# Optimization experiments

Measured on AMD Instinct MI355X. Metric: run time of the kernel, lower is better.

## Reference

```python
import jax, jax.numpy as jnp
import numpy as np

N, E = 50000, 800000
F_IN, HID, H, LBL = 512, 16, 8, 40
HC = HID * H  # 128
BN_EPS = 1e-5
ELU_ALPHA = 0.2
NEG_SLOPE = 0.2


def setup_inputs() -> dict:
    key = jax.random.key(0)
    ks = jax.random.split(key, 32)
    inp = {}
    inp['x'] = jax.random.normal(ks[0], (N, F_IN), dtype=jnp.float32)
    inp['edge_index'] = jax.random.randint(ks[1], (2, E), 0, N, dtype=jnp.int32)
    # layer 0: F_IN -> (H, HID), concat
    inp['W0'] = jax.random.normal(ks[2], (F_IN, HC), dtype=jnp.float32) * 0.05
    inp['as0'] = jax.random.normal(ks[3], (H, HID), dtype=jnp.float32) * 0.1
    inp['ad0'] = jax.random.normal(ks[4], (H, HID), dtype=jnp.float32) * 0.1
    inp['b0'] = jnp.zeros((HC,), jnp.float32)
    inp['g0'] = jnp.ones((HC,), jnp.float32)
    inp['be0'] = jnp.zeros((HC,), jnp.float32)
    inp['rm0'] = jnp.zeros((HC,), jnp.float32)
    inp['rv0'] = jnp.ones((HC,), jnp.float32)
    # layer 1: HC -> (H, HID), concat
    inp['W1'] = jax.random.normal(ks[5], (HC, HC), dtype=jnp.float32) * 0.1
    inp['as1'] = jax.random.normal(ks[6], (H, HID), dtype=jnp.float32) * 0.1
    inp['ad1'] = jax.random.normal(ks[7], (H, HID), dtype=jnp.float32) * 0.1
    inp['b1'] = jnp.zeros((HC,), jnp.float32)
    inp['g1'] = jnp.ones((HC,), jnp.float32)
    inp['be1'] = jnp.zeros((HC,), jnp.float32)
    inp['rm1'] = jnp.zeros((HC,), jnp.float32)
    inp['rv1'] = jnp.ones((HC,), jnp.float32)
    # layer 2: HC -> (1, LBL), mean (concat=False)
    inp['W2'] = jax.random.normal(ks[8], (HC, LBL), dtype=jnp.float32) * 0.1
    inp['as2'] = jax.random.normal(ks[9], (1, LBL), dtype=jnp.float32) * 0.1
    inp['ad2'] = jax.random.normal(ks[10], (1, LBL), dtype=jnp.float32) * 0.1
    inp['b2'] = jnp.zeros((LBL,), jnp.float32)
    return inp


def _gat_conv(xf, src, dst, W, a_src, a_dst, b, heads, out_ch, concat):
    # PyG GATConv (eval): linear -> per-head attn logits -> segment softmax over dst -> scatter-add
    n = xf.shape[0]
    h = (xf @ W).reshape(n, heads, out_ch)            # [N,H,C]
    alpha_s = jnp.einsum('nhc,hc->nh', h, a_src)      # [N,H]
    alpha_d = jnp.einsum('nhc,hc->nh', h, a_dst)
    e = jax.nn.leaky_relu(alpha_s[src] + alpha_d[dst], NEG_SLOPE)  # [Etot,H]
    m = jax.ops.segment_max(e, dst, num_segments=n)
    e = jnp.exp(e - m[dst])
    s = jax.ops.segment_sum(e, dst, num_segments=n)
    alpha = e / (s[dst] + 1e-16)                      # [Etot,H]
    msg = alpha[:, :, None] * h[src]                  # [Etot,H,C]
    out = jax.ops.segment_sum(msg, dst, num_segments=n)  # [N,H,C]
    out = out.reshape(n, heads * out_ch) if concat else out.mean(axis=1)
    return out + b


def _bn_elu(xf, g, be, rm, rv):
    y = (xf - rm) * (g * jax.lax.rsqrt(rv + BN_EPS)) + be
    return jnp.where(y > 0, y, ELU_ALPHA * jnp.expm1(y))


def reference(x, edge_index, W0, as0, ad0, b0, g0, be0, rm0, rv0,
              W1, as1, ad1, b1, g1, be1, rm1, rv1, W2, as2, ad2, b2):
    n = x.shape[0]
    # add self-loops (PyG GATConv default add_self_loops=True)
    loops = jnp.arange(n, dtype=edge_index.dtype)
    src = jnp.concatenate([edge_index[0], loops])
    dst = jnp.concatenate([edge_index[1], loops])
    h = _gat_conv(x, src, dst, W0, as0, ad0, b0, H, HID, True)
    h = _bn_elu(h, g0, be0, rm0, rv0)
    h = _gat_conv(h, src, dst, W1, as1, ad1, b1, H, HID, True)
    h = _bn_elu(h, g1, be1, rm1, rv1)
    out = _gat_conv(h, src, dst, W2, as2, ad2, b2, 1, LBL, False)
    return out
```

## Files before the change

### kernel.cpp

```cpp
#include <hip/hip_runtime.h>
#include <hip/hip_bf16.h>
#include <cstdint>
#include <cstddef>

#define NN 50000
#define EE 800000
#define FIN 512
#define HIDC 16
#define NH 8
#define HCH 128
#define NLBL 40
#define NLBLP 48
#define ETOT (EE + NN)
#define NEG_SLOPE 0.2f
#define ELU_A 0.2f
#define BN_EPS 1e-5f
#define SCH 8192
#define NCHK 7

typedef __attribute__((ext_vector_type(8))) short bf16x8;
typedef __attribute__((ext_vector_type(4))) short bf16x4;
typedef __attribute__((ext_vector_type(4))) float f32x4;

__device__ inline short f2b(float f) {
    __hip_bfloat16 h = __float2bfloat16(f);
    return *reinterpret_cast<short*>(&h);
}
__device__ inline float blo(unsigned int u) {
    union { unsigned int u; float f; } v; v.u = u << 16; return v.f;
}
__device__ inline float bhi(unsigned int u) {
    union { unsigned int u; float f; } v; v.u = u & 0xffff0000u; return v.f;
}

__global__ __launch_bounds__(256) void k_prep(const float* __restrict__ W0, short* __restrict__ Wt0,
                                              const float* __restrict__ W1, short* __restrict__ Wt1,
                                              const float* __restrict__ W2, short* __restrict__ Wt2,
                                              const int* __restrict__ ei, int* __restrict__ deg,
                                              const float* __restrict__ x, short* __restrict__ xc)
{
    int b = blockIdx.x;
    int tid = threadIdx.x;
    if (b < 256) {
        int idx = b * 256 + tid;
        int n = idx >> 9, k = idx & 511;
        Wt0[idx] = f2b(W0[(size_t)k * HCH + n]);
        return;
    }
    b -= 256;
    if (b < 64) {
        int idx = b * 256 + tid;
        int n = idx >> 7, k = idx & 127;
        Wt1[idx] = f2b(W1[(size_t)k * HCH + n]);
        return;
    }
    b -= 64;
    if (b < 24) {
        int idx = b * 256 + tid;
        int n = idx >> 7, k = idx & 127;
        Wt2[idx] = f2b(n < NLBL ? W2[(size_t)k * NLBL + n] : 0.f);
        return;
    }
    b -= 24;
    if (b < 3321) {
        int e = b * 256 + tid;
        if (e < ETOT) {
            int dst = (e < EE) ? ei[EE + e] : (e - EE);
            atomicAdd(&deg[dst], 1);
        }
        return;
    }
    b -= 3321;
    {
        int t = b * 256 + tid;
        if (t < NN * (FIN / 8)) {
            int idx = t * 8;
            int row = idx >> 9;
            int ko  = idx & 511;
            int c   = ko >> 7;
            int kk  = ko & 127;
            const float4* p = (const float4*)(x + (size_t)row * FIN + ko);
            float4 v0 = p[0], v1 = p[1];
            bf16x8 w;
            w[0] = f2b(v0.x); w[1] = f2b(v0.y); w[2] = f2b(v0.z); w[3] = f2b(v0.w);
            w[4] = f2b(v1.x); w[5] = f2b(v1.y); w[6] = f2b(v1.z); w[7] = f2b(v1.w);
            *(bf16x8*)(xc + ((size_t)c * NN + row) * 128 + kk) = w;
        }
    }
}

__global__ __launch_bounds__(1024) void k_scan1(const int* __restrict__ deg,
                                                int* __restrict__ row_ptr,
                                                int* __restrict__ tot)
{
    __shared__ int sm[1024];
    int b = blockIdx.x, tid = threadIdx.x;
    int i0 = b * SCH + tid * 8;
    int v[8];
    int s = 0;
    #pragma unroll
    for (int j = 0; j < 8; ++j) {
        int i = i0 + j;
        v[j] = (i < NN) ? deg[i] : 0;
        s += v[j];
    }
    sm[tid] = s;
    __syncthreads();
    for (int ofs = 1; ofs < 1024; ofs <<= 1) {
        int t = (tid >= ofs) ? sm[tid - ofs] : 0;
        __syncthreads();
        sm[tid] += t;
        __syncthreads();
    }
    int excl = sm[tid] - s;
    #pragma unroll
    for (int j = 0; j < 8; ++j) {
        int i = i0 + j;
        if (i < NN) row_ptr[i] = excl;
        excl += v[j];
    }
    if (tid == 1023) tot[b] = sm[1023];
}

__global__ __launch_bounds__(64) void k_scan2(const int* __restrict__ tot,
                                              int* __restrict__ totp,
                                              int* __restrict__ row_ptr)
{
    if (threadIdx.x == 0) {
        int run = 0;
        for (int i = 0; i < NCHK; ++i) { totp[i] = run; run += tot[i]; }
        row_ptr[NN] = run;
    }
}

__global__ __launch_bounds__(256) void k_scan3(int* __restrict__ row_ptr,
                                               int* __restrict__ cursor,
                                               const int* __restrict__ totp)
{
    int i = blockIdx.x * 256 + threadIdx.x;
    if (i < NN) {
        int v = row_ptr[i] + totp[i / SCH];
        row_ptr[i] = v;
        cursor[i] = v;
    }
}

__global__ __launch_bounds__(256) void k_scatter(const int* __restrict__ ei,
                                                 int* __restrict__ cursor,
                                                 int* __restrict__ csr_src)
{
    int e = blockIdx.x * blockDim.x + threadIdx.x;
    if (e >= ETOT) return;
    int src, dst;
    if (e < EE) { src = ei[e]; dst = ei[EE + e]; }
    else        { src = dst = e - EE; }
    int pos = atomicAdd(&cursor[dst], 1);
    csr_src[pos] = src;
}

template<int KDIM, bool CHUNK_MAJOR>
__global__ __launch_bounds__(512, 4) void k_gemm2(const short* __restrict__ Ab,
                                                  const short* __restrict__ Wt,
                                                  short* __restrict__ C,
                                                  int M,
                                                  const float* __restrict__ a_s,
                                                  const float* __restrict__ a_d,
                                                  float* __restrict__ as_o,
                                                  float* __restrict__ ad_o)
{
    constexpr int KCH  = 128;
    constexpr int NCH  = KDIM / KCH;
    constexpr int LROW = KCH + 8;
    __shared__ short As[64 * LROW];
    __shared__ short Bs[128 * LROW];

    const int tid  = threadIdx.x;
    const int wv   = tid >> 6;
    const int lane = tid & 63;
    const int quad = lane >> 4;
    const int col  = lane & 15;
    const int wr   = wv >> 1;
    const int wn   = wv & 1;
    const int rowbase = blockIdx.x * 64;

    bf16x8 pab[2];
    bf16x8 pb[4];

    auto loadA = [&](int c) {
        #pragma unroll
        for (int r = 0; r < 2; ++r) {
            int gr = rowbase + r * 32 + (tid >> 4);
            gr = gr < M ? gr : M - 1;
            size_t base = CHUNK_MAJOR ? ((size_t)c * M + gr) * KCH
                                      : (size_t)gr * KDIM + (size_t)c * KCH;
            pab[r] = *(const bf16x8*)(Ab + base + (tid & 15) * 8);
        }
    };
    auto loadB = [&](int c) {
        #pragma unroll
        for (int r = 0; r < 4; ++r) {
            int n = r * 32 + (tid >> 4);
            pb[r] = *(const bf16x8*)(Wt + (size_t)n * KDIM + (size_t)c * KCH + (tid & 15) * 8);
        }
    };
    auto writeAB = [&]() {
        #pragma unroll
        for (int r = 0; r < 2; ++r) {
            int row = r * 32 + (tid >> 4);
            *(bf16x8*)(As + row * LROW + (tid & 15) * 8) = pab[r];
        }
        #pragma unroll
        for (int r = 0; r < 4; ++r) {
            int n = r * 32 + (tid >> 4);
            *(bf16x8*)(Bs + n * LROW + (tid & 15) * 8) = pb[r];
        }
    };

    f32x4 acc[4];
    #pragma unroll
    for (int t = 0; t < 4; ++t) acc[t] = (f32x4){0.f, 0.f, 0.f, 0.f};

    loadA(0); loadB(0);

    for (int c = 0; c < NCH; ++c) {
        writeAB();
        __syncthreads();
        if (c + 1 < NCH) { loadA(c + 1); loadB(c + 1); }
        #pragma unroll
        for (int s = 0; s < KCH / 32; ++s) {
            bf16x8 af = *(const bf16x8*)(As + (wr * 16 + col) * LROW + s * 32 + quad * 8);
            #pragma unroll
            for (int t = 0; t < 4; ++t) {
                bf16x8 bf = *(const bf16x8*)(Bs + (wn * 64 + t * 16 + col) * LROW + s * 32 + quad * 8);
                acc[t] = __builtin_amdgcn_mfma_f32_16x16x32_bf16(af, bf, acc[t], 0, 0, 0);
            }
        }
        if (c + 1 < NCH) __syncthreads();
    }

    const int mb = rowbase + wr * 16 + quad * 4;

    #pragma unroll
    for (int t = 0; t < 4; ++t) {
        int cc = wn * 64 + t * 16 + col;
        #pragma unroll
        for (int r = 0; r < 4; ++r) {
            int m = mb + r;
            if (m < M) C[(size_t)m * HCH + cc] = f2b(acc[t][r]);
        }
    }

    #pragma unroll
    for (int t = 0; t < 4; ++t) {
        int hh = wn * 4 + t;
        float ws = a_s[hh * HIDC + col];
        float wd = a_d[hh * HIDC + col];
        #pragma unroll
        for (int r = 0; r < 4; ++r) {
            float vs = acc[t][r] * ws;
            float vd = acc[t][r] * wd;
            vs += __shfl_xor(vs, 1);  vd += __shfl_xor(vd, 1);
            vs += __shfl_xor(vs, 2);  vd += __shfl_xor(vd, 2);
            vs += __shfl_xor(vs, 4);  vd += __shfl_xor(vd, 4);
            vs += __shfl_xor(vs, 8);  vd += __shfl_xor(vd, 8);
            int m = mb + r;
            if (col == 0 && m < M) {
                as_o[m * NH + hh] = vs;
                ad_o[m * NH + hh] = vd;
            }
        }
    }
}

template<int KDIM, int NTILES>
__global__ __launch_bounds__(256) void k_gemm_lds(const short* __restrict__ Ab,
                                                  const short* __restrict__ Wt,
                                                  short* __restrict__ C,
                                                  int M, int N,
                                                  const float* __restrict__ a_s2,
                                                  const float* __restrict__ a_d2,
                                                  float* __restrict__ as_o,
                                                  float* __restrict__ ad_o)
{
    constexpr int NFULL = NTILES * 16;
    constexpr int KCH = 128;
    constexpr int NK = KDIM / 32;
    constexpr int NCH = KDIM / KCH;
    constexpr int LROW = KCH + 8;
    __shared__ short Bs[NFULL * LROW];

    const int tid  = threadIdx.x;
    const int wave = tid >> 6;
    const int lane = tid & 63;
    const int quad = lane >> 4;
    const int col  = lane & 15;
    const int row  = blockIdx.x * 64 + wave * 16 + col;
    const int arow = row < M ? row : M - 1;

    f32x4 acc[NTILES];
    #pragma unroll
    for (int t = 0; t < NTILES; ++t) acc[t] = (f32x4){0.f, 0.f, 0.f, 0.f};

    bf16x8 arB[4];
    auto pf = [&](int ks) {
        if (ks >= NK) return;
        arB[ks & 3] = *(const bf16x8*)(Ab + (size_t)arow * KDIM + ks * 32 + quad * 8);
    };
    pf(0); pf(1); pf(2); pf(3);

    for (int c = 0; c < NCH; ++c) {
        const int k0 = c * KCH;
        constexpr int TOT8 = NFULL * (KCH / 8);
        #pragma unroll
        for (int i = tid; i < TOT8; i += 256) {
            int n  = i >> 4;
            int kk = i & 15;
            bf16x8 v = *(const bf16x8*)(Wt + (size_t)n * KDIM + k0 + kk * 8);
            *(bf16x8*)(Bs + n * LROW + kk * 8) = v;
        }
        __syncthreads();
        #pragma unroll
        for (int s = 0; s < KCH / 32; ++s) {
            const int ks = c * (KCH / 32) + s;
            bf16x8 afrag = arB[ks & 3];
            pf(ks + 4);
            #pragma unroll
            for (int t = 0; t < NTILES; ++t) {
                bf16x8 bfrag = *(const bf16x8*)(Bs + (t * 16 + col) * LROW + s * 32 + quad * 8);
                acc[t] = __builtin_amdgcn_mfma_f32_16x16x32_bf16(afrag, bfrag, acc[t], 0, 0, 0);
            }
        }
        if (c + 1 < NCH) __syncthreads();
    }

    const int mbase = blockIdx.x * 64 + wave * 16 + quad * 4;
    #pragma unroll
    for (int t = 0; t < NTILES; ++t) {
        int cc = t * 16 + col;
        if (cc < N) {
            #pragma unroll
            for (int r = 0; r < 4; ++r) {
                int m = mbase + r;
                if (m < M) C[(size_t)m * N + cc] = f2b(acc[t][r]);
            }
        }
    }

    float vs[4] = {0.f, 0.f, 0.f, 0.f};
    float vd[4] = {0.f, 0.f, 0.f, 0.f};
    #pragma unroll
    for (int t = 0; t < NTILES; ++t) {
        int cc = t * 16 + col;
        float ws = cc < NLBL ? a_s2[cc] : 0.f;
        float wd = cc < NLBL ? a_d2[cc] : 0.f;
        #pragma unroll
        for (int r = 0; r < 4; ++r) {
            vs[r] += acc[t][r] * ws;
            vd[r] += acc[t][r] * wd;
        }
    }
    #pragma unroll
    for (int r = 0; r < 4; ++r) {
        float s = vs[r], d = vd[r];
        s += __shfl_xor(s, 1);  d += __shfl_xor(d, 1);
        s += __shfl_xor(s, 2);  d += __shfl_xor(d, 2);
        s += __shfl_xor(s, 4);  d += __shfl_xor(d, 4);
        s += __shfl_xor(s, 8);  d += __shfl_xor(d, 8);
        int m = mbase + r;
        if (col == 0 && m < M) {
            as_o[m] = s;
            ad_o[m] = d;
        }
    }
}

__global__ __launch_bounds__(256) void k_agg(const int* __restrict__ row_ptr,
                                             const int* __restrict__ csr_src,
                                             const unsigned short* __restrict__ h,
                                             const float* __restrict__ as,
                                             const float* __restrict__ ad,
                                             const float* __restrict__ b,
                                             const float* __restrict__ g,
                                             const float* __restrict__ be,
                                             const float* __restrict__ rm,
                                             const float* __restrict__ rv,
                                             short* __restrict__ out)
{
    int n = blockIdx.x * 4 + (threadIdx.x >> 6);
    if (n >= NN) return;
    int lane = threadIdx.x & 63;
    int half = lane >> 5;
    int c4 = lane & 31;
    int hh = c4 >> 2;
    float adv = ad[n * NH + hh];
    float a0 = 0.f, a1 = 0.f, a2 = 0.f, a3 = 0.f, sw = 0.f;
    int jb = row_ptr[n], je = row_ptr[n + 1];
    int j = jb + half;
    for (; j + 14 < je; j += 16) {
        int s[8];
        #pragma unroll
        for (int q = 0; q < 8; ++q) s[q] = csr_src[j + 2 * q];
        float l[8];
        uint2 u[8];
        #pragma unroll
        for (int q = 0; q < 8; ++q) {
            l[q] = as[s[q] * NH + hh] + adv;
            u[q] = *(const uint2*)(h + (size_t)s[q] * HCH + 4 * c4);
        }
        #pragma unroll
        for (int q = 0; q < 8; ++q) {
            float lq = l[q] > 0.f ? l[q] : NEG_SLOPE * l[q];
            float w = __expf(lq);
            sw += w;
            a0 += w * blo(u[q].x);
            a1 += w * bhi(u[q].x);
            a2 += w * blo(u[q].y);
            a3 += w * bhi(u[q].y);
        }
    }
    for (; j + 6 < je; j += 8) {
        int s0 = csr_src[j];
        int s1 = csr_src[j + 2];
        int s2 = csr_src[j + 4];
        int s3 = csr_src[j + 6];
        float l0 = as[s0 * NH + hh] + adv;
        float l1 = as[s1 * NH + hh] + adv;
        float l2 = as[s2 * NH + hh] + adv;
        float l3 = as[s3 * NH + hh] + adv;
        uint2 u0 = *(const uint2*)(h + (size_t)s0 * HCH + 4 * c4);
        uint2 u1 = *(const uint2*)(h + (size_t)s1 * HCH + 4 * c4);
        uint2 u2 = *(const uint2*)(h + (size_t)s2 * HCH + 4 * c4);
        uint2 u3 = *(const uint2*)(h + (size_t)s3 * HCH + 4 * c4);
        l0 = l0 > 0.f ? l0 : NEG_SLOPE * l0;
        l1 = l1 > 0.f ? l1 : NEG_SLOPE * l1;
        l2 = l2 > 0.f ? l2 : NEG_SLOPE * l2;
        l3 = l3 > 0.f ? l3 : NEG_SLOPE * l3;
        float w0 = __expf(l0), w1 = __expf(l1), w2 = __expf(l2), w3 = __expf(l3);
        sw += (w0 + w1) + (w2 + w3);
        a0 += w0 * blo(u0.x) + w1 * blo(u1.x) + w2 * blo(u2.x) + w3 * blo(u3.x);
        a1 += w0 * bhi(u0.x) + w1 * bhi(u1.x) + w2 * bhi(u2.x) + w3 * bhi(u3.x);
        a2 += w0 * blo(u0.y) + w1 * blo(u1.y) + w2 * blo(u2.y) + w3 * blo(u3.y);
        a3 += w0 * bhi(u0.y) + w1 * bhi(u1.y) + w2 * bhi(u2.y) + w3 * bhi(u3.y);
    }
    for (; j < je; j += 2) {
        int s0 = csr_src[j];
        float l0 = as[s0 * NH + hh] + adv;
        uint2 u0 = *(const uint2*)(h + (size_t)s0 * HCH + 4 * c4);
        l0 = l0 > 0.f ? l0 : NEG_SLOPE * l0;
        float w0 = __expf(l0);
        sw += w0;
        a0 += w0 * blo(u0.x);
        a1 += w0 * bhi(u0.x);
        a2 += w0 * blo(u0.y);
        a3 += w0 * bhi(u0.y);
    }
    a0 += __shfl_down(a0, 32);
    a1 += __shfl_down(a1, 32);
    a2 += __shfl_down(a2, 32);
    a3 += __shfl_down(a3, 32);
    sw += __shfl_down(sw, 32);
    if (half == 0) {
        int c = 4 * c4;
        float inv = 1.f / (sw + 1e-16f);
        float4 bv  = *(const float4*)(b + c);
        float4 gv  = *(const float4*)(g + c);
        float4 bev = *(const float4*)(be + c);
        float4 rmv = *(const float4*)(rm + c);
        float4 rvv = *(const float4*)(rv + c);
        float r0 = a0 * inv + bv.x;
        float r1 = a1 * inv + bv.y;
        float r2 = a2 * inv + bv.z;
        float r3 = a3 * inv + bv.w;
        r0 = (r0 - rmv.x) * (gv.x * rsqrtf(rvv.x + BN_EPS)) + bev.x;
        r1 = (r1 - rmv.y) * (gv.y * rsqrtf(rvv.y + BN_EPS)) + bev.y;
        r2 = (r2 - rmv.z) * (gv.z * rsqrtf(rvv.z + BN_EPS)) + bev.z;
        r3 = (r3 - rmv.w) * (gv.w * rsqrtf(rvv.w + BN_EPS)) + bev.w;
        r0 = r0 > 0.f ? r0 : ELU_A * expm1f(r0);
        r1 = r1 > 0.f ? r1 : ELU_A * expm1f(r1);
        r2 = r2 > 0.f ? r2 : ELU_A * expm1f(r2);
        r3 = r3 > 0.f ? r3 : ELU_A * expm1f(r3);
        unsigned int lo = (unsigned int)(unsigned short)f2b(r0) |
                          ((unsigned int)(unsigned short)f2b(r1) << 16);
        unsigned int hi = (unsigned int)(unsigned short)f2b(r2) |
                          ((unsigned int)(unsigned short)f2b(r3) << 16);
        *(uint2*)(out + (size_t)n * HCH + c) = make_uint2(lo, hi);
    }
}

__global__ __launch_bounds__(256) void k_agg2(const int* __restrict__ row_ptr,
                                              const int* __restrict__ csr_src,
                                              const unsigned short* __restrict__ h2,
                                              const float* __restrict__ as,
                                              const float* __restrict__ ad,
                                              const float* __restrict__ b,
                                              float* __restrict__ out)
{
    int n = blockIdx.x * 4 + (threadIdx.x >> 6);
    if (n >= NN) return;
    int lane = threadIdx.x & 63;
    int half = lane >> 5;
    int c2 = lane & 31;
    bool act = c2 < 20;
    int coff = act ? 2 * c2 : 0;
    float adv = ad[n];
    float acc0 = 0.f, acc1 = 0.f, sw = 0.f;
    int jb = row_ptr[n], je = row_ptr[n + 1];
    int j = jb + half;
    for (; j + 14 < je; j += 16) {
        int s[8];
        #pragma unroll
        for (int q = 0; q < 8; ++q) s[q] = csr_src[j + 2 * q];
        float l[8];
        unsigned int u[8];
        #pragma unroll
        for (int q = 0; q < 8; ++q) {
            l[q] = as[s[q]] + adv;
            u[q] = *(const unsigned int*)(h2 + (size_t)s[q] * NLBL + coff);
        }
        #pragma unroll
        for (int q = 0; q < 8; ++q) {
            float lq = l[q] > 0.f ? l[q] : NEG_SLOPE * l[q];
            float w = __expf(lq);
            sw += w;
            if (act) {
                acc0 += w * blo(u[q]);
                acc1 += w * bhi(u[q]);
            }
        }
    }
    for (; j + 6 < je; j += 8) {
        int s0 = csr_src[j];
        int s1 = csr_src[j + 2];
        int s2 = csr_src[j + 4];
        int s3 = csr_src[j + 6];
        float l0 = as[s0] + adv;
        float l1 = as[s1] + adv;
        float l2 = as[s2] + adv;
        float l3 = as[s3] + adv;
        unsigned int u0 = *(const unsigned int*)(h2 + (size_t)s0 * NLBL + coff);
        unsigned int u1 = *(const unsigned int*)(h2 + (size_t)s1 * NLBL + coff);
        unsigned int u2 = *(const unsigned int*)(h2 + (size_t)s2 * NLBL + coff);
        unsigned int u3 = *(const unsigned int*)(h2 + (size_t)s3 * NLBL + coff);
        l0 = l0 > 0.f ? l0 : NEG_SLOPE * l0;
        l1 = l1 > 0.f ? l1 : NEG_SLOPE * l1;
        l2 = l2 > 0.f ? l2 : NEG_SLOPE * l2;
        l3 = l3 > 0.f ? l3 : NEG_SLOPE * l3;
        float w0 = __expf(l0), w1 = __expf(l1), w2 = __expf(l2), w3 = __expf(l3);
        sw += (w0 + w1) + (w2 + w3);
        if (act) {
            acc0 += w0 * blo(u0) + w1 * blo(u1) + w2 * blo(u2) + w3 * blo(u3);
            acc1 += w0 * bhi(u0) + w1 * bhi(u1) + w2 * bhi(u2) + w3 * bhi(u3);
        }
    }
    for (; j < je; j += 2) {
        int s = csr_src[j];
        float l = as[s] + adv;
        unsigned int u = *(const unsigned int*)(h2 + (size_t)s * NLBL + coff);
        l = l > 0.f ? l : NEG_SLOPE * l;
        float w = __expf(l);
        sw += w;
        if (act) {
            acc0 += w * blo(u);
            acc1 += w * bhi(u);
        }
    }
    float acc0b = __shfl_down(acc0, 32);
    float acc1b = __shfl_down(acc1, 32);
    float swb   = __shfl_down(sw, 32);
    if (half == 0 && act) {
        acc0 += acc0b; acc1 += acc1b; sw += swb;
        float inv = 1.f / (sw + 1e-16f);
        out[(size_t)n * NLBL + 2 * c2]     = acc0 * inv + b[2 * c2];
        out[(size_t)n * NLBL + 2 * c2 + 1] = acc1 * inv + b[2 * c2 + 1];
    }
}

extern "C" void kernel_launch(void* const* d_in, const int* in_sizes, int n_in,
                              void* d_out, int out_size, void* d_ws, size_t ws_size,
                              hipStream_t stream)
{
    const float* x   = (const float*)d_in[0];
    const int*   ei  = (const int*)d_in[1];
    const float* W0  = (const float*)d_in[2];
    const float* as0 = (const float*)d_in[3];
    const float* ad0 = (const float*)d_in[4];
    const float* b0  = (const float*)d_in[5];
    const float* g0  = (const float*)d_in[6];
    const float* be0 = (const float*)d_in[7];
    const float* rm0 = (const float*)d_in[8];
    const float* rv0 = (const float*)d_in[9];
    const float* W1  = (const float*)d_in[10];
    const float* as1 = (const float*)d_in[11];
    const float* ad1 = (const float*)d_in[12];
    const float* b1  = (const float*)d_in[13];
    const float* g1  = (const float*)d_in[14];
    const float* be1 = (const float*)d_in[15];
    const float* rm1 = (const float*)d_in[16];
    const float* rv1 = (const float*)d_in[17];
    const float* W2  = (const float*)d_in[18];
    const float* a_s2 = (const float*)d_in[19];
    const float* a_d2 = (const float*)d_in[20];
    const float* b2  = (const float*)d_in[21];
    float* out = (float*)d_out;

    char* ws = (char*)d_ws;
    size_t off = 0;
    auto alloc = [&](size_t bytes) {
        void* p = (void*)(ws + off);
        off += (bytes + 255) & ~(size_t)255;
        return p;
    };
    short* hbuf   = (short*)alloc((size_t)NN * HCH * 2);
    short* fbuf   = (short*)alloc((size_t)NN * HCH * 2);
    short* xc     = (short*)alloc((size_t)4 * NN * 128 * 2);
    float* asb    = (float*)alloc((size_t)NN * NH * 4);
    float* adb    = (float*)alloc((size_t)NN * NH * 4);
    int*   deg    = (int*)alloc((size_t)NN * 4);
    int*   rowp   = (int*)alloc((size_t)(NN + 1) * 4);
    int*   cursor = (int*)alloc((size_t)NN * 4);
    int*   csrs   = (int*)alloc((size_t)ETOT * 4);
    short* Wt0    = (short*)alloc((size_t)HCH * FIN * 2);
    short* Wt1    = (short*)alloc((size_t)HCH * HCH * 2);
    short* Wt2    = (short*)alloc((size_t)NLBLP * HCH * 2);
    int*   tot    = (int*)alloc(64 * 4);
    int*   totp   = (int*)alloc(64 * 4);
    short* h2     = hbuf;

    const int T = 256;
    const int gN4 = (NN + 3) / 4;
    const int gM  = (NN + 63) / 64;
    const int gHist = (ETOT + T - 1) / T;
    const int gConv = (NN * (FIN / 8) + T - 1) / T;
    const int gPrep = 256 + 64 + 24 + gHist + gConv;
    const int gE  = gHist;

    hipMemsetAsync(deg, 0, (size_t)NN * 4, stream);
    k_prep<<<gPrep, T, 0, stream>>>(W0, Wt0, W1, Wt1, W2, Wt2, ei, deg, x, xc);

    k_scan1<<<NCHK, 1024, 0, stream>>>(deg, rowp, tot);
    k_scan2<<<1, 64, 0, stream>>>(tot, totp, rowp);
    k_scan3<<<(NN + T - 1) / T, T, 0, stream>>>(rowp, cursor, totp);
    k_scatter<<<gE, T, 0, stream>>>(ei, cursor, csrs);

    k_gemm2<FIN, true><<<gM, 512, 0, stream>>>(xc, Wt0, hbuf, NN, as0, ad0, asb, adb);
    k_agg<<<gN4, T, 0, stream>>>(rowp, csrs, (const unsigned short*)hbuf, asb, adb,
                                 b0, g0, be0, rm0, rv0, fbuf);

    k_gemm2<HCH, false><<<gM, 512, 0, stream>>>(fbuf, Wt1, hbuf, NN, as1, ad1, asb, adb);
    k_agg<<<gN4, T, 0, stream>>>(rowp, csrs, (const unsigned short*)hbuf, asb, adb,
                                 b1, g1, be1, rm1, rv1, fbuf);

    k_gemm_lds<HCH, 3><<<gM, T, 0, stream>>>(fbuf, Wt2, h2, NN, NLBL,
                                             a_s2, a_d2, asb, adb);
    k_agg2<<<gN4, T, 0, stream>>>(rowp, csrs, (const unsigned short*)h2, asb, adb, b2, out);
}
```

Measured before the change: 460.5 us.

## Fuse fp32-to-bf16 input conversion into first-layer GEMM A loads

Removes the separate conversion pass that wrote a chunk-major bf16 copy of x. The layer-0 GEMM now reads fp32 x directly, converts to bf16 while staging into LDS, and prefetches all K chunks of A into registers up front. This cuts the extra write and read of the converted input. In exchange it raises register pressure in the GEMM and loses per-chunk double buffering of A.

```diff
diff --git a/kernel.cpp b/kernel.cpp
--- a/kernel.cpp
+++ b/kernel.cpp
@@ -36,8 +36,7 @@
 __global__ __launch_bounds__(256) void k_prep(const float* __restrict__ W0, short* __restrict__ Wt0,
                                               const float* __restrict__ W1, short* __restrict__ Wt1,
                                               const float* __restrict__ W2, short* __restrict__ Wt2,
-                                              const int* __restrict__ ei, int* __restrict__ deg,
-                                              const float* __restrict__ x, short* __restrict__ xc)
+                                              const int* __restrict__ ei, int* __restrict__ deg)
 {
     int b = blockIdx.x;
     int tid = threadIdx.x;
@@ -62,29 +61,11 @@
         return;
     }
     b -= 24;
-    if (b < 3321) {
+    {
         int e = b * 256 + tid;
         if (e < ETOT) {
             int dst = (e < EE) ? ei[EE + e] : (e - EE);
             atomicAdd(&deg[dst], 1);
-        }
-        return;
-    }
-    b -= 3321;
-    {
-        int t = b * 256 + tid;
-        if (t < NN * (FIN / 8)) {
-            int idx = t * 8;
-            int row = idx >> 9;
-            int ko  = idx & 511;
-            int c   = ko >> 7;
-            int kk  = ko & 127;
-            const float4* p = (const float4*)(x + (size_t)row * FIN + ko);
-            float4 v0 = p[0], v1 = p[1];
-            bf16x8 w;
-            w[0] = f2b(v0.x); w[1] = f2b(v0.y); w[2] = f2b(v0.z); w[3] = f2b(v0.w);
-            w[4] = f2b(v1.x); w[5] = f2b(v1.y); w[6] = f2b(v1.z); w[7] = f2b(v1.w);
-            *(bf16x8*)(xc + ((size_t)c * NN + row) * 128 + kk) = w;
         }
     }
 }
@@ -158,8 +139,8 @@
     csr_src[pos] = src;
 }
 
-template<int KDIM, bool CHUNK_MAJOR>
-__global__ __launch_bounds__(512, 4) void k_gemm2(const short* __restrict__ Ab,
+template<int KDIM, bool A_BF16>
+__global__ __launch_bounds__(512, 4) void k_gemm2(const void* __restrict__ Ap,
                                                   const short* __restrict__ Wt,
                                                   short* __restrict__ C,
                                                   int M,
@@ -183,49 +164,76 @@
     const int wn   = wv & 1;
     const int rowbase = blockIdx.x * 64;
 
+    const float* Af = (const float*)Ap;
+    const short* Ab = (const short*)Ap;
+
+    float4 pa[NCH][4];
     bf16x8 pab[2];
     bf16x8 pb[4];
 
-    auto loadA = [&](int c) {
+    auto loadB = [&](int c) {
+        #pragma unroll
+        for (int r = 0; r < 4; ++r) {
+            int n = r * 32 + (tid >> 4);
+            pb[r] = *(const bf16x8*)(Wt + (size_t)n * KDIM + (size_t)c * KCH + (tid & 15) * 8);
+        }
+    };
+
+    if constexpr (A_BF16) {
         #pragma unroll
         for (int r = 0; r < 2; ++r) {
             int gr = rowbase + r * 32 + (tid >> 4);
             gr = gr < M ? gr : M - 1;
-            size_t base = CHUNK_MAJOR ? ((size_t)c * M + gr) * KCH
-                                      : (size_t)gr * KDIM + (size_t)c * KCH;
-            pab[r] = *(const bf16x8*)(Ab + base + (tid & 15) * 8);
-        }
-    };
-    auto loadB = [&](int c) {
+            pab[r] = *(const bf16x8*)(Ab + (size_t)gr * KDIM + (tid & 15) * 8);
+        }
+        loadB(0);
+    } else {
         #pragma unroll
         for (int r = 0; r < 4; ++r) {
-            int n = r * 32 + (tid >> 4);
-            pb[r] = *(const bf16x8*)(Wt + (size_t)n * KDIM + (size_t)c * KCH + (tid & 15) * 8);
-        }
-    };
-    auto writeAB = [&]() {
-        #pragma unroll
-        for (int r = 0; r < 2; ++r) {
-            int row = r * 32 + (tid >> 4);
-            *(bf16x8*)(As + row * LROW + (tid & 15) * 8) = pab[r];
+            int gr = rowbase + r * 16 + (tid >> 5);
+            gr = gr < M ? gr : M - 1;
+            pa[0][r] = *(const float4*)(Af + (size_t)gr * KDIM + (tid & 31) * 4);
+        }
+        loadB(0);
+        #pragma unroll
+        for (int c = 1; c < NCH; ++c)
+            #pragma unroll
+            for (int r = 0; r < 4; ++r) {
+                int gr = rowbase + r * 16 + (tid >> 5);
+                gr = gr < M ? gr : M - 1;
+                pa[c][r] = *(const float4*)(Af + (size_t)gr * KDIM + c * KCH + (tid & 31) * 4);
+            }
+    }
+
+    f32x4 acc[4];
+    #pragma unroll
+    for (int t = 0; t < 4; ++t) acc[t] = (f32x4){0.f, 0.f, 0.f, 0.f};
+
+    #pragma unroll
+    for (int c = 0; c < NCH; ++c) {
+        if constexpr (A_BF16) {
+            #pragma unroll
+            for (int r = 0; r < 2; ++r) {
+                int row = r * 32 + (tid >> 4);
+                *(bf16x8*)(As + row * LROW + (tid & 15) * 8) = pab[r];
+            }
+        } else {
+            #pragma unroll
+            for (int r = 0; r < 4; ++r) {
+                int row = r * 16 + (tid >> 5);
+                bf16x4 w;
+                w[0] = f2b(pa[c][r].x); w[1] = f2b(pa[c][r].y);
+                w[2] = f2b(pa[c][r].z); w[3] = f2b(pa[c][r].w);
+                *(bf16x4*)(As + row * LROW + (tid & 31) * 4) = w;
+            }
         }
         #pragma unroll
         for (int r = 0; r < 4; ++r) {
             int n = r * 32 + (tid >> 4);
             *(bf16x8*)(Bs + n * LROW + (tid & 15) * 8) = pb[r];
         }
-    };
-
-    f32x4 acc[4];
-    #pragma unroll
-    for (int t = 0; t < 4; ++t) acc[t] = (f32x4){0.f, 0.f, 0.f, 0.f};
-
-    loadA(0); loadB(0);
-
-    for (int c = 0; c < NCH; ++c) {
-        writeAB();
         __syncthreads();
-        if (c + 1 < NCH) { loadA(c + 1); loadB(c + 1); }
+        if (c + 1 < NCH) loadB(c + 1);
         #pragma unroll
         for (int s = 0; s < KCH / 32; ++s) {
             bf16x8 af = *(const bf16x8*)(As + (wr * 16 + col) * LROW + s * 32 + quad * 8);
@@ -612,7 +620,6 @@
     };
     short* hbuf   = (short*)alloc((size_t)NN * HCH * 2);
     short* fbuf   = (short*)alloc((size_t)NN * HCH * 2);
-    short* xc     = (short*)alloc((size_t)4 * NN * 128 * 2);
     float* asb    = (float*)alloc((size_t)NN * NH * 4);
     float* adb    = (float*)alloc((size_t)NN * NH * 4);
     int*   deg    = (int*)alloc((size_t)NN * 4);
@@ -629,24 +636,22 @@
     const int T = 256;
     const int gN4 = (NN + 3) / 4;
     const int gM  = (NN + 63) / 64;
-    const int gHist = (ETOT + T - 1) / T;
-    const int gConv = (NN * (FIN / 8) + T - 1) / T;
-    const int gPrep = 256 + 64 + 24 + gHist + gConv;
-    const int gE  = gHist;
+    const int gE  = (ETOT + T - 1) / T;
+    const int gPrep = 256 + 64 + 24 + gE;
 
     hipMemsetAsync(deg, 0, (size_t)NN * 4, stream);
-    k_prep<<<gPrep, T, 0, stream>>>(W0, Wt0, W1, Wt1, W2, Wt2, ei, deg, x, xc);
+    k_prep<<<gPrep, T, 0, stream>>>(W0, Wt0, W1, Wt1, W2, Wt2, ei, deg);
 
     k_scan1<<<NCHK, 1024, 0, stream>>>(deg, rowp, tot);
     k_scan2<<<1, 64, 0, stream>>>(tot, totp, rowp);
     k_scan3<<<(NN + T - 1) / T, T, 0, stream>>>(rowp, cursor, totp);
     k_scatter<<<gE, T, 0, stream>>>(ei, cursor, csrs);
 
-    k_gemm2<FIN, true><<<gM, 512, 0, stream>>>(xc, Wt0, hbuf, NN, as0, ad0, asb, adb);
+    k_gemm2<FIN, false><<<gM, 512, 0, stream>>>(x, Wt0, hbuf, NN, as0, ad0, asb, adb);
     k_agg<<<gN4, T, 0, stream>>>(rowp, csrs, (const unsigned short*)hbuf, asb, adb,
                                  b0, g0, be0, rm0, rv0, fbuf);
 
-    k_gemm2<HCH, false><<<gM, 512, 0, stream>>>(fbuf, Wt1, hbuf, NN, as1, ad1, asb, adb);
+    k_gemm2<HCH, true><<<gM, 512, 0, stream>>>(fbuf, Wt1, hbuf, NN, as1, ad1, asb, adb);
     k_agg<<<gN4, T, 0, stream>>>(rowp, csrs, (const unsigned short*)hbuf, asb, adb,
                                  b1, g1, be1, rm1, rv1, fbuf);
 
```

After: 464.6 us. No clear change (+0.9%).
